# Kernel tuning notes

Measured on AMD Instinct MI355X. Metric: run time of the kernel, lower is better.

## Reference

```python
import jax, jax.numpy as jnp
import numpy as np

N_NODES = 50000
EPS_NORM = 1e-12
EPS_ENT = 1e-8

def _l2norm(x):
    # torch.nn.functional.normalize: x / clamp(||x||, min=1e-12)
    n = jnp.sqrt(jnp.sum(x * x, axis=-1, keepdims=True))
    return x / jnp.maximum(n, EPS_NORM)

def _layer(hidden, src, dst, edge_type, multi_emb, proto_emb):
    # hidden: [N,H]; multi_emb: [R,P,H]; proto_emb: [P,H]
    inp_j = hidden[src]                          # [E,H] gather
    rel_basis = multi_emb[edge_type]             # [E,P,H] gather
    sims = jnp.einsum('eh,ph->ep', _l2norm(inp_j), _l2norm(proto_emb))  # cosine sim [E,P]
    proto_proba = jax.nn.softmax(sims, axis=1)   # [E,P]
    msg = jnp.einsum('ep,eph->eh', proto_proba, rel_basis)              # [E,H]
    ent = -jnp.sum(proto_proba * jnp.log(proto_proba + EPS_ENT), axis=1)  # [E]
    logits = -ent
    # scatter_softmax over destination index
    seg_max = jax.ops.segment_max(logits, dst, num_segments=N_NODES)
    ex = jnp.exp(logits - seg_max[dst])
    denom = jax.ops.segment_sum(ex, dst, num_segments=N_NODES)
    attn = ex / denom[dst]                       # [E]
    out = jax.ops.segment_sum(attn[:, None] * msg, dst, num_segments=N_NODES)  # [N,H]
    return out

def setup_inputs() -> dict:
    key = jax.random.key(0)
    ks = jax.random.split(key, 6)
    E = 800000
    H, R, P, L = 128, 18, 18, 3  # num_layers=4 -> 3 NBFCluttr layers
    edge_index = jax.random.randint(ks[0], (2, E), 0, N_NODES, dtype=jnp.int64) if jax.config.read('jax_enable_x64') else jax.random.randint(ks[0], (2, E), 0, N_NODES, dtype=jnp.int32)
    edge_type = jax.random.randint(ks[1], (E,), 0, R, dtype=edge_index.dtype)
    tail_indices = jax.random.randint(ks[2], (1024,), 0, N_NODES, dtype=edge_index.dtype)
    multi_embeddings = jax.random.uniform(ks[3], (L, R, P, H), dtype=jnp.float32)
    proto_embeddings = jax.random.uniform(ks[4], (L, P, H), dtype=jnp.float32)
    source_embedding = jax.random.uniform(ks[5], (H,), dtype=jnp.float32)
    return {"edge_index": edge_index, "edge_type": edge_type, "tail_indices": tail_indices,
            "multi_embeddings": multi_embeddings, "proto_embeddings": proto_embeddings,
            "source_embedding": source_embedding}

def reference(edge_index, edge_type, tail_indices, multi_embeddings, proto_embeddings, source_embedding):
    src, dst = edge_index[0], edge_index[1]
    H = source_embedding.shape[0]
    # boundary condition: source node gets source_embedding, rest zero
    hidden = jnp.zeros((N_NODES, H), dtype=source_embedding.dtype).at[0].set(source_embedding)
    L = multi_embeddings.shape[0]
    for l in range(L):  # small fixed loop over structurally distinct layers
        hidden = _layer(hidden, src, dst, edge_type, multi_embeddings[l], proto_embeddings[l])
    # apply_classifier, eval_mode=True, use_mlp_classifier=False -> cosine sims to last layer prototypes
    out_emb = hidden[tail_indices]               # [B,H]
    sims = jnp.einsum('nh,ph->np', _l2norm(out_emb), _l2norm(proto_embeddings[-1]))
    return sims  # gumbel_softmax_sample with eval_mode=True returns logits unchanged
```

## Files before the change

### kernel.cpp

```cpp
#include <hip/hip_runtime.h>
#include <hip/hip_bf16.h>


#define N_NODES 50000
#define H 128
#define P 18
#define RP 324
#define KPAD 352
#define K0PAD 32
#define ELLW 64
#define NPART 8
#define NODES_PER_PART 6250
#define PREP_MAIN_BLOCKS 384
#define PREP_PN_BLOCKS 14
#define PREP_GS_BLOCKS 162
#define N0CAP 1024

typedef _Float16 half8 __attribute__((ext_vector_type(8)));
typedef _Float16 half2v __attribute__((ext_vector_type(2)));
typedef float floatx4 __attribute__((ext_vector_type(4)));

__global__ __launch_bounds__(256) void ell_kernel(const int* __restrict__ src,
                                                  const int* __restrict__ dst,
                                                  const int* __restrict__ etype,
                                                  unsigned* __restrict__ cur,
                                                  unsigned* __restrict__ ep,
                                                  unsigned* __restrict__ n0list, int E) {
  int part = blockIdx.x & (NPART - 1);
  int i = (blockIdx.x >> 3) * 256 + threadIdx.x;
  if (i >= E) return;
  int d = dst[i];
  int lo = part * NODES_PER_PART;
  if (d < lo || d >= lo + NODES_PER_PART) return;
  int s = src[i];
  int r = etype[i];
  unsigned pos = atomicAdd(&cur[d], 1u);
  if (pos < ELLW)
    ep[(size_t)d * ELLW + pos] = (unsigned)s | ((unsigned)r << 20);
  if (s == 0) {
    unsigned ix = atomicAdd(&cur[N_NODES], 1u);
    if (ix < N0CAP) n0list[ix] = (unsigned)d | ((unsigned)r << 20);
  }
}

__global__ __launch_bounds__(256) void prep_kernel(const float* __restrict__ multi,
                                                   const float* __restrict__ proto,
                                                   const float* __restrict__ semb,
                                                   float* __restrict__ pN,
                                                   _Float16* __restrict__ Btg,
                                                   _Float16* __restrict__ Btl0,
                                                   _Float16* __restrict__ BtD,
                                                   float* __restrict__ GS,
                                                   unsigned* __restrict__ cur) {
  int bid = blockIdx.x;
  if (bid >= PREP_MAIN_BLOCKS + PREP_PN_BLOCKS) {
    int wave = threadIdx.x >> 6, lane = threadIdx.x & 63;
    int pi = (bid - PREP_MAIN_BLOCKS - PREP_PN_BLOCKS) * 4 + wave;
    if (pi >= 648) return;
    float pr = 1.f / 18.f, ent0 = 0.f;
#pragma unroll
    for (int p = 0; p < P; p++) ent0 -= pr * __logf(pr + 1e-8f);
    float qc = __expf(-ent0) * pr;
    bool isG = pi < 324;
    int rr = isG ? pi / P : (pi - 324) / P;
    int cc = isG ? pi - rr * P : (pi - 324) - rr * P;
    float ca = 0.f, cb = 0.f;
#pragma unroll
    for (int q2 = 0; q2 < P; q2++) {
      ca += multi[(rr * P + q2) * H + lane];
      cb += multi[(rr * P + q2) * H + lane + 64];
    }
    ca *= qc; cb *= qc;
    float xa, xb, rn = 0.f;
    if (isG) {
      xa = proto[(P + cc) * H + lane];
      xb = proto[(P + cc) * H + lane + 64];
      rn = xa * xa + xb * xb;
    } else {
      xa = 0.f; xb = 0.f;
#pragma unroll
      for (int q2 = 0; q2 < P; q2++) {
        xa += multi[(cc * P + q2) * H + lane];
        xb += multi[(cc * P + q2) * H + lane + 64];
      }
      xa *= qc; xb *= qc;
    }
    float dotp = ca * xa + cb * xb;
    for (int m = 32; m > 0; m >>= 1) {
      dotp += __shfl_xor(dotp, m, 64);
      rn += __shfl_xor(rn, m, 64);
    }
    float val = isG ? dotp / fmaxf(sqrtf(rn), 1e-12f) : dotp;
    if (lane == 0) GS[pi] = val;
    return;
  }
  if (bid >= PREP_MAIN_BLOCKS) {
    int wave = threadIdx.x >> 6, l = threadIdx.x & 63;
    int row = (bid - PREP_MAIN_BLOCKS) * 4 + wave;
    if (row >= 54) return;
    float a = proto[row * H + l], b = proto[row * H + 64 + l];
    float ss = a * a + b * b;
    for (int m = 32; m > 0; m >>= 1) ss += __shfl_xor(ss, m, 64);
    float inv = 1.f / fmaxf(sqrtf(ss), 1e-12f);
    pN[row * H + l] = a * inv;
    pN[row * H + 64 + l] = b * inv;
    return;
  }
  int idx = bid * 256 + threadIdx.x;
  if (idx <= N_NODES) cur[idx] = 0u;
  if (idx < 2 * H * KPAD) {
    int l = idx / (H * KPAD), rem = idx - l * (H * KPAD);
    int h = rem / KPAD, k = rem - h * KPAD;
    const float* B = multi + (size_t)(l + 1) * RP * H;
    Btg[idx] = (k < RP) ? (_Float16)B[k * H + h] : (_Float16)0.f;
    return;
  }
  int idx2 = idx - 2 * H * KPAD;
  if (idx2 >= H * 64) return;
  int h = idx2 >> 6, k = idx2 & 63;
  float s0 = semb[k], s1 = semb[k + 64];
  float ssq = s0 * s0 + s1 * s1;
  float dq[P];
#pragma unroll
  for (int p = 0; p < P; p++) {
    float a = proto[p * H + k], b = proto[p * H + 64 + k];
    float rn = a * a + b * b;
    for (int m = 32; m > 0; m >>= 1) rn += __shfl_xor(rn, m, 64);
    float rinv = 1.f / fmaxf(sqrtf(rn), 1e-12f);
    dq[p] = (s0 * a + s1 * b) * rinv;
  }
  for (int m = 1; m <= 32; m <<= 1) {
    ssq += __shfl_xor(ssq, m, 64);
#pragma unroll
    for (int p = 0; p < P; p++) dq[p] += __shfl_xor(dq[p], m, 64);
  }
  float inv = 1.f / fmaxf(sqrtf(ssq), 1e-12f);
  float sum = 0.f;
#pragma unroll
  for (int p = 0; p < P; p++) {
    dq[p] = __expf(dq[p] * inv - 1.f);
    sum += dq[p];
  }
  float isum = 1.f / sum, ent = 0.f;
#pragma unroll
  for (int p = 0; p < P; p++) {
    dq[p] *= isum;
    ent -= dq[p] * __logf(dq[p] + 1e-8f);
  }
  float w = __expf(-ent);
  float pr = 1.f / 18.f, ent0 = 0.f;
#pragma unroll
  for (int p = 0; p < P; p++) ent0 -= pr * __logf(pr + 1e-8f);
  float qc = __expf(-ent0) * pr;
  if (k < K0PAD) {
    float v = 0.f;
    if (k < P) {
#pragma unroll
      for (int p = 0; p < P; p++) v += qc * multi[(k * P + p) * H + h];
    }
    Btl0[h * K0PAD + k] = (_Float16)v;
  } else if (k < K0PAD + P) {
    int r = k - K0PAD;
    float v = 0.f;
#pragma unroll
    for (int p = 0; p < P; p++) v += (w * dq[p] - qc) * multi[(r * P + p) * H + h];
    BtD[r * H + h] = (_Float16)v;
  }
}

__global__ __launch_bounds__(256) void histq_kernel(const unsigned* __restrict__ ep,
                                                    const unsigned* __restrict__ cur,
                                                    const float* __restrict__ GS,
                                                    _Float16* __restrict__ q, int n) {
  __shared__ float gs[648];
  for (int i = threadIdx.x; i < 648; i += 256) gs[i] = GS[i];
  __syncthreads();
  int wave = threadIdx.x >> 6, lane = threadIdx.x & 63;
  int nd = blockIdx.x * 4 + wave;
  if (nd >= n) return;
  int cnt = (int)cur[nd];
  if (cnt > ELLW) cnt = ELLW;
  bool a = lane < cnt;
  unsigned pk = a ? ep[(size_t)nd * ELLW + lane] : 0xFFFFFFFFu;
  int r = (int)(pk >> 20);
  float creg = 0.f;
#pragma unroll
  for (int rr = 0; rr < P; rr++) {
    unsigned long long m = __ballot(a && (r == rr));
    if (lane == rr) creg = (float)__popcll(m);
  }
  float dot = 0.f, t = 0.f;
#pragma unroll
  for (int rr = 0; rr < P; rr++) {
    float c = __shfl(creg, rr, 64);
    if (lane < P) {
      dot += c * gs[rr * P + lane];
      t += c * gs[324 + rr * P + lane];
    }
  }
  float u = (lane < P) ? creg * t : 0.f;
  for (int m = 1; m <= 16; m <<= 1) u += __shfl_xor(u, m, 32);
  float ss = u;
  float inv = 1.f / fmaxf(sqrtf(ss), 1e-12f);
  float e = (lane < P) ? __expf(dot * inv - 1.f) : 0.f;
  float sum = e;
  for (int m = 1; m <= 16; m <<= 1) sum += __shfl_xor(sum, m, 32);
  float prb = e / sum;
  float term = (lane < P) ? prb * __logf(prb + 1e-8f) : 0.f;
  float ent = term;
  for (int m = 1; m <= 16; m <<= 1) ent += __shfl_xor(ent, m, 32);
  float w = __expf(ent);
  if (lane < P) q[(size_t)nd * P + lane] = (_Float16)(w * prb);
}

__global__ __launch_bounds__(256) void patch_kernel(const unsigned* __restrict__ cur,
                                                    const unsigned* __restrict__ n0list,
                                                    const unsigned* __restrict__ ep,
                                                    const _Float16* __restrict__ Btl0,
                                                    const _Float16* __restrict__ BtD,
                                                    const float* __restrict__ pN,
                                                    _Float16* __restrict__ q) {
  int n0 = (int)cur[N_NODES];
  if (n0 > N0CAP) n0 = N0CAP;
  int wave = threadIdx.x >> 6, lane = threadIdx.x & 63;
  int e = blockIdx.x * 4 + wave;
  if (e >= n0) return;
  unsigned pe = n0list[e];
  int d = (int)(pe & 0xFFFFFu);
  for (int e2 = 0; e2 < e; e2++)
    if ((int)(n0list[e2] & 0xFFFFFu) == d) return;
  int cnt = (int)cur[d];
  if (cnt > ELLW) cnt = ELLW;
  bool a = lane < cnt;
  unsigned pk2 = a ? ep[(size_t)d * ELLW + lane] : 0xFFFFFFFFu;
  int rr0 = (int)(pk2 >> 20);
  float creg = 0.f;
#pragma unroll
  for (int rr = 0; rr < P; rr++) {
    unsigned long long m = __ballot(a && (rr0 == rr));
    if (lane == rr) creg = (float)__popcll(m);
  }
  float ya = 0.f, yb = 0.f;
#pragma unroll
  for (int rr = 0; rr < P; rr++) {
    float c = __shfl(creg, rr, 64);
    ya += c * (float)Btl0[lane * K0PAD + rr];
    yb += c * (float)Btl0[(lane + 64) * K0PAD + rr];
  }
  for (int e2 = e; e2 < n0; e2++) {
    unsigned p2 = n0list[e2];
    if ((int)(p2 & 0xFFFFFu) != d) continue;
    int r2 = (int)(p2 >> 20);
    ya += (float)BtD[r2 * H + lane];
    yb += (float)BtD[r2 * H + lane + 64];
  }
  float ss = ya * ya + yb * yb;
  float dot[P];
#pragma unroll
  for (int p = 0; p < P; p++) dot[p] = ya * pN[p * H + lane] + yb * pN[p * H + lane + 64];
  for (int m = 1; m <= 32; m <<= 1) {
    ss += __shfl_xor(ss, m, 64);
#pragma unroll
    for (int p = 0; p < P; p++) dot[p] += __shfl_xor(dot[p], m, 64);
  }
  float inv = 1.f / fmaxf(sqrtf(ss), 1e-12f);
  float sum = 0.f;
#pragma unroll
  for (int p = 0; p < P; p++) {
    dot[p] = __expf(dot[p] * inv - 1.f);
    sum += dot[p];
  }
  float isum = 1.f / sum, ent = 0.f;
#pragma unroll
  for (int p = 0; p < P; p++) {
    dot[p] *= isum;
    ent -= dot[p] * __logf(dot[p] + 1e-8f);
  }
  float w = __expf(-ent);
  if (lane < P) q[(size_t)d * P + lane] = (_Float16)(w * dot[lane]);
}

__global__ __launch_bounds__(256) void scatter_kernel(const unsigned* __restrict__ ep,
                                                      const unsigned* __restrict__ cur,
                                                      const _Float16* __restrict__ q,
                                                      const int* __restrict__ tl,
                                                      _Float16* __restrict__ M, int n) {
  __shared__ float sl[4][3 * RP];
  int wave = threadIdx.x >> 6, lane = threadIdx.x & 63;
  int t = blockIdx.x * 4 + wave;
  float* s0 = sl[wave];
  for (int i = lane; i < 3 * RP; i += 64) s0[i] = 0.f;
  int sub = lane / 18;
  int j = lane - sub * 18;
  bool act = (sub < 3) && (t < n);
  int cnt = 0;
  size_t b = 0;
  if (t < n) {
    int nd = tl ? tl[t] : t;
    b = (size_t)nd * ELLW;
    cnt = (int)cur[nd];
    if (cnt > ELLW) cnt = ELLW;
  }
  float* ms = s0 + (sub < 3 ? sub : 0) * RP;
  for (int it = 0; it < cnt; it += 18) {
    bool aa[6];
    unsigned pk[6];
    float qv[6];
#pragma unroll
    for (int u = 0; u < 6; u++) {
      int e = it + 3 * u + sub;
      aa[u] = act && (e < cnt);
      pk[u] = aa[u] ? ep[b + e] : 0u;
    }
#pragma unroll
    for (int u = 0; u < 6; u++)
      qv[u] = aa[u] ? (float)q[(size_t)(pk[u] & 0xFFFFFu) * P + j] : 0.f;
#pragma unroll
    for (int u = 0; u < 6; u++)
      if (aa[u]) ms[(pk[u] >> 20) * P + j] += qv[u];
  }
  if (t < n) {
    for (int wd = lane; wd < RP / 2; wd += 64) {
      float2 x0 = *(const float2*)(s0 + 2 * wd);
      float2 x1 = *(const float2*)(s0 + RP + 2 * wd);
      float2 x2 = *(const float2*)(s0 + 2 * RP + 2 * wd);
      half2v hv;
      hv[0] = (_Float16)(x0.x + x1.x + x2.x);
      hv[1] = (_Float16)(x0.y + x1.y + x2.y);
      *(half2v*)(M + (size_t)t * KPAD + 2 * wd) = hv;
    }
    for (int wd = RP / 2 + lane; wd < KPAD / 2; wd += 64) {
      half2v z = {};
      *(half2v*)(M + (size_t)t * KPAD + 2 * wd) = z;
    }
  }
}

template <int MODE>
__global__ __launch_bounds__(256) void gemm_kernel(const _Float16* __restrict__ M,
                                                   const _Float16* __restrict__ Bt,
                                                   const float* __restrict__ pN,
                                                   void* __restrict__ out_ptr, int n,
                                                   int kpad) {
  __shared__ float smem_f[64 * 132];
  _Float16* As = (_Float16*)smem_f;
  _Float16* Bs = (_Float16*)(smem_f + 1024);
  int tid = threadIdx.x;
  int wave = tid >> 6, lane = tid & 63;
  int m15 = lane & 15, quad = lane >> 4;
  int n0 = blockIdx.x * 64;
  floatx4 acc[4][2] = {};

  __shared__ float pns[4 * P * 36];
  for (int i = tid; i < 4 * P * 32; i += 256) {
    int s = i / (P * 32), r = i - s * (P * 32);
    int p = r >> 5, kk = r & 31;
    pns[s * (P * 36) + p * 36 + kk] = pN[p * H + s * 32 + kk];
  }

  for (int kt = 0; kt < (kpad >> 5); kt++) {
    int k0 = kt * 32;
    __syncthreads();
    {
      int row = tid >> 2, kc = (tid & 3) * 8;
      int gr = n0 + row;
      half8 v = {};
      if (gr < n) v = *(const half8*)(M + (size_t)gr * kpad + k0 + kc);
      *(half8*)(As + row * 32 + kc) = v;
    }
    {
      int col = tid >> 1, kc = (tid & 1) * 16;
      const _Float16* srcp = Bt + (size_t)col * kpad + k0 + kc;
      *(half8*)(Bs + col * 32 + kc) = *(const half8*)srcp;
      *(half8*)(Bs + col * 32 + kc + 8) = *(const half8*)(srcp + 8);
    }
    __syncthreads();
    half8 bfrag0 = *(const half8*)(Bs + (wave * 32 + m15) * 32 + quad * 8);
    half8 bfrag1 = *(const half8*)(Bs + (wave * 32 + 16 + m15) * 32 + quad * 8);
#pragma unroll
    for (int mt = 0; mt < 4; mt++) {
      half8 afrag = *(const half8*)(As + (mt * 16 + m15) * 32 + quad * 8);
      acc[mt][0] = __builtin_amdgcn_mfma_f32_16x16x32_f16(afrag, bfrag0, acc[mt][0], 0, 0, 0);
      acc[mt][1] = __builtin_amdgcn_mfma_f32_16x16x32_f16(afrag, bfrag1, acc[mt][1], 0, 0, 0);
    }
  }
  __syncthreads();
#pragma unroll
  for (int mt = 0; mt < 4; mt++)
#pragma unroll
    for (int c = 0; c < 2; c++)
#pragma unroll
      for (int reg = 0; reg < 4; reg++)
        smem_f[(mt * 16 + quad * 4 + reg) * 132 + wave * 32 + c * 16 + m15] = acc[mt][c][reg];
  __syncthreads();
  int node = tid >> 2, sub = tid & 3;
  int gnode = n0 + node;
  const float* trow = smem_f + node * 132 + sub * 32;
  const float* ps = pns + sub * (P * 36);
  float ss = 0.f;
  float dot[P];
#pragma unroll
  for (int p = 0; p < P; p++) dot[p] = 0.f;
#pragma unroll
  for (int k4 = 0; k4 < 8; k4++) {
    float4 y = *(const float4*)(trow + k4 * 4);
    ss += y.x * y.x + y.y * y.y + y.z * y.z + y.w * y.w;
#pragma unroll
    for (int p = 0; p < P; p++) {
      float4 b = *(const float4*)(ps + p * 36 + k4 * 4);
      dot[p] += y.x * b.x + y.y * b.y + y.z * b.z + y.w * b.w;
    }
  }
  for (int m = 1; m <= 2; m <<= 1) {
    ss += __shfl_xor(ss, m, 64);
#pragma unroll
    for (int p = 0; p < P; p++) dot[p] += __shfl_xor(dot[p], m, 64);
  }
  if (gnode < n) {
    float inv = 1.f / fmaxf(sqrtf(ss), 1e-12f);
    if (MODE == 1) {
      float* outp = (float*)out_ptr;
      for (int p = sub; p < P; p += 4) outp[(size_t)gnode * P + p] = dot[p] * inv;
    } else {
      float sum = 0.f;
#pragma unroll
      for (int p = 0; p < P; p++) {
        dot[p] = __expf(dot[p] * inv - 1.f);
        sum += dot[p];
      }
      float isum = 1.f / sum, ent = 0.f;
#pragma unroll
      for (int p = 0; p < P; p++) {
        dot[p] *= isum;
        ent -= dot[p] * __logf(dot[p] + 1e-8f);
      }
      float w = __expf(-ent);
      _Float16* qp = (_Float16*)out_ptr;
      for (int p = sub; p < P; p += 4) qp[(size_t)gnode * P + p] = (_Float16)(w * dot[p]);
    }
  }
}

extern "C" void kernel_launch(void* const* d_in, const int* in_sizes, int n_in,
                              void* d_out, int out_size, void* d_ws, size_t ws_size,
                              hipStream_t stream) {
  const int* eidx = (const int*)d_in[0];
  int E = in_sizes[0] / 2;
  const int* src = eidx;
  const int* dst = eidx + E;
  const int* etype = (const int*)d_in[1];
  const int* tails = (const int*)d_in[2];
  int T = in_sizes[2];
  const float* multi = (const float*)d_in[3];
  const float* proto = (const float*)d_in[4];
  const float* semb = (const float*)d_in[5];
  float* out = (float*)d_out;

  char* w = (char*)d_ws;
  auto alloc = [&](size_t bytes) {
    char* p = w;
    w += (bytes + 255) & ~(size_t)255;
    return p;
  };
  _Float16* q = (_Float16*)alloc((size_t)N_NODES * P * 2);
  float* pNs = (float*)alloc((size_t)3 * P * H * 4);
  float* GS = (float*)alloc((size_t)648 * 4);
  _Float16* Mg = (_Float16*)alloc((size_t)N_NODES * KPAD * 2);
  _Float16* Btg = (_Float16*)alloc((size_t)2 * H * KPAD * 2);
  _Float16* Btl0 = (_Float16*)alloc((size_t)H * K0PAD * 2);
  _Float16* BtD = (_Float16*)alloc((size_t)P * H * 2);
  unsigned* cur = (unsigned*)alloc((size_t)(N_NODES + 1) * 4);
  unsigned* n0list = (unsigned*)alloc((size_t)N0CAP * 4);
  unsigned* ep = (unsigned*)alloc((size_t)N_NODES * ELLW * 4);

  int eb = (E + 255) / 256;

  prep_kernel<<<PREP_MAIN_BLOCKS + PREP_PN_BLOCKS + PREP_GS_BLOCKS, 256, 0, stream>>>(
      multi, proto, semb, pNs, Btg, Btl0, BtD, GS, cur);

  ell_kernel<<<eb * NPART, 256, 0, stream>>>(src, dst, etype, cur, ep, n0list, E);

  histq_kernel<<<(N_NODES + 3) / 4, 256, 0, stream>>>(ep, cur, GS, q, N_NODES);
  patch_kernel<<<(N0CAP + 3) / 4, 256, 0, stream>>>(cur, n0list, ep, Btl0, BtD,
                                                    pNs + (size_t)1 * P * H, q);

  scatter_kernel<<<(N_NODES + 3) / 4, 256, 0, stream>>>(ep, cur, q, nullptr, Mg, N_NODES);
  gemm_kernel<0><<<(N_NODES + 63) / 64, 256, 0, stream>>>(Mg, Btg, pNs + (size_t)2 * P * H, q,
                                                          N_NODES, KPAD);

  scatter_kernel<<<(T + 3) / 4, 256, 0, stream>>>(ep, cur, q, tails, Mg, T);
  gemm_kernel<1><<<(T + 63) / 64, 256, 0, stream>>>(Mg, Btg + (size_t)H * KPAD,
                                                    pNs + (size_t)2 * P * H, out, T, KPAD);
}
```

Before: 230.9 us.

## Restrict penultimate layer to in-neighbors of tail nodes

Adds a need_kernel that marks and compacts the distinct source nodes feeding the tail nodes. The layer-2 scatter and GEMM then run only over that compacted list, with the GEMM writing q through an index map, instead of over all 50000 nodes. Effective sizes are read from a device counter, so blocks past the live count exit early. This cuts most of the full-graph scatter and GEMM work. In exchange it adds a small extra kernel with atomics, and it silently drops nodes if more than NEED_CAP distinct neighbors are needed.

```diff
diff --git a/kernel.cpp b/kernel.cpp
--- a/kernel.cpp
+++ b/kernel.cpp
@@ -15,6 +15,7 @@
 #define PREP_PN_BLOCKS 14
 #define PREP_GS_BLOCKS 162
 #define N0CAP 1024
+#define NEED_CAP 20480
 
 typedef _Float16 half8 __attribute__((ext_vector_type(8)));
 typedef _Float16 half2v __attribute__((ext_vector_type(2)));
@@ -43,6 +44,26 @@
   }
 }
 
+__global__ __launch_bounds__(256) void need_kernel(const int* __restrict__ tl,
+                                                   const unsigned* __restrict__ ep,
+                                                   unsigned* __restrict__ cur,
+                                                   unsigned* __restrict__ nflag,
+                                                   unsigned* __restrict__ needlist, int T) {
+  int wave = threadIdx.x >> 6, lane = threadIdx.x & 63;
+  int t = blockIdx.x * 4 + wave;
+  if (t >= T) return;
+  int nd = tl[t];
+  int cnt = (int)cur[nd];
+  if (cnt > ELLW) cnt = ELLW;
+  if (lane < cnt) {
+    unsigned s = ep[(size_t)nd * ELLW + lane] & 0xFFFFFu;
+    if (atomicExch(&nflag[s], 1u) == 0u) {
+      unsigned ix = atomicAdd(&cur[N_NODES + 1], 1u);
+      if (ix < NEED_CAP) needlist[ix] = s;
+    }
+  }
+}
+
 __global__ __launch_bounds__(256) void prep_kernel(const float* __restrict__ multi,
                                                    const float* __restrict__ proto,
                                                    const float* __restrict__ semb,
@@ -51,7 +72,8 @@
                                                    _Float16* __restrict__ Btl0,
                                                    _Float16* __restrict__ BtD,
                                                    float* __restrict__ GS,
-                                                   unsigned* __restrict__ cur) {
+                                                   unsigned* __restrict__ cur,
+                                                   unsigned* __restrict__ nflag) {
   int bid = blockIdx.x;
   if (bid >= PREP_MAIN_BLOCKS + PREP_PN_BLOCKS) {
     int wave = threadIdx.x >> 6, lane = threadIdx.x & 63;
@@ -107,7 +129,8 @@
     return;
   }
   int idx = bid * 256 + threadIdx.x;
-  if (idx <= N_NODES) cur[idx] = 0u;
+  if (idx <= N_NODES + 1) cur[idx] = 0u;
+  if (idx < N_NODES) nflag[idx] = 0u;
   if (idx < 2 * H * KPAD) {
     int l = idx / (H * KPAD), rem = idx - l * (H * KPAD);
     int h = rem / KPAD, k = rem - h * KPAD;
@@ -284,18 +307,24 @@
                                                       const unsigned* __restrict__ cur,
                                                       const _Float16* __restrict__ q,
                                                       const int* __restrict__ tl,
+                                                      const unsigned* __restrict__ dc,
                                                       _Float16* __restrict__ M, int n) {
   __shared__ float sl[4][3 * RP];
   int wave = threadIdx.x >> 6, lane = threadIdx.x & 63;
   int t = blockIdx.x * 4 + wave;
+  int neff = n;
+  if (dc) {
+    int c = (int)dc[0];
+    if (c < neff) neff = c;
+  }
   float* s0 = sl[wave];
   for (int i = lane; i < 3 * RP; i += 64) s0[i] = 0.f;
   int sub = lane / 18;
   int j = lane - sub * 18;
-  bool act = (sub < 3) && (t < n);
+  bool act = (sub < 3) && (t < neff);
   int cnt = 0;
   size_t b = 0;
-  if (t < n) {
+  if (t < neff) {
     int nd = tl ? tl[t] : t;
     b = (size_t)nd * ELLW;
     cnt = (int)cur[nd];
@@ -319,7 +348,7 @@
     for (int u = 0; u < 6; u++)
       if (aa[u]) ms[(pk[u] >> 20) * P + j] += qv[u];
   }
-  if (t < n) {
+  if (t < neff) {
     for (int wd = lane; wd < RP / 2; wd += 64) {
       float2 x0 = *(const float2*)(s0 + 2 * wd);
       float2 x1 = *(const float2*)(s0 + RP + 2 * wd);
@@ -340,15 +369,23 @@
 __global__ __launch_bounds__(256) void gemm_kernel(const _Float16* __restrict__ M,
                                                    const _Float16* __restrict__ Bt,
                                                    const float* __restrict__ pN,
+                                                   const int* __restrict__ map,
+                                                   const unsigned* __restrict__ dc,
                                                    void* __restrict__ out_ptr, int n,
                                                    int kpad) {
+  int neff = n;
+  if (dc) {
+    int c = (int)dc[0];
+    if (c < neff) neff = c;
+  }
+  int n0 = blockIdx.x * 64;
+  if (n0 >= neff) return;
   __shared__ float smem_f[64 * 132];
   _Float16* As = (_Float16*)smem_f;
   _Float16* Bs = (_Float16*)(smem_f + 1024);
   int tid = threadIdx.x;
   int wave = tid >> 6, lane = tid & 63;
   int m15 = lane & 15, quad = lane >> 4;
-  int n0 = blockIdx.x * 64;
   floatx4 acc[4][2] = {};
 
   __shared__ float pns[4 * P * 36];
@@ -365,7 +402,7 @@
       int row = tid >> 2, kc = (tid & 3) * 8;
       int gr = n0 + row;
       half8 v = {};
-      if (gr < n) v = *(const half8*)(M + (size_t)gr * kpad + k0 + kc);
+      if (gr < neff) v = *(const half8*)(M + (size_t)gr * kpad + k0 + kc);
       *(half8*)(As + row * 32 + kc) = v;
     }
     {
@@ -416,7 +453,7 @@
 #pragma unroll
     for (int p = 0; p < P; p++) dot[p] += __shfl_xor(dot[p], m, 64);
   }
-  if (gnode < n) {
+  if (gnode < neff) {
     float inv = 1.f / fmaxf(sqrtf(ss), 1e-12f);
     if (MODE == 1) {
       float* outp = (float*)out_ptr;
@@ -435,8 +472,9 @@
         ent -= dot[p] * __logf(dot[p] + 1e-8f);
       }
       float w = __expf(-ent);
+      int gout = map ? map[gnode] : gnode;
       _Float16* qp = (_Float16*)out_ptr;
-      for (int p = sub; p < P; p += 4) qp[(size_t)gnode * P + p] = (_Float16)(w * dot[p]);
+      for (int p = sub; p < P; p += 4) qp[(size_t)gout * P + p] = (_Float16)(w * dot[p]);
     }
   }
 }
@@ -469,14 +507,17 @@
   _Float16* Btg = (_Float16*)alloc((size_t)2 * H * KPAD * 2);
   _Float16* Btl0 = (_Float16*)alloc((size_t)H * K0PAD * 2);
   _Float16* BtD = (_Float16*)alloc((size_t)P * H * 2);
-  unsigned* cur = (unsigned*)alloc((size_t)(N_NODES + 1) * 4);
+  unsigned* cur = (unsigned*)alloc((size_t)(N_NODES + 2) * 4);
   unsigned* n0list = (unsigned*)alloc((size_t)N0CAP * 4);
+  unsigned* nflag = (unsigned*)alloc((size_t)N_NODES * 4);
+  unsigned* needlist = (unsigned*)alloc((size_t)NEED_CAP * 4);
   unsigned* ep = (unsigned*)alloc((size_t)N_NODES * ELLW * 4);
 
   int eb = (E + 255) / 256;
+  const unsigned* needcnt = cur + N_NODES + 1;
 
   prep_kernel<<<PREP_MAIN_BLOCKS + PREP_PN_BLOCKS + PREP_GS_BLOCKS, 256, 0, stream>>>(
-      multi, proto, semb, pNs, Btg, Btl0, BtD, GS, cur);
+      multi, proto, semb, pNs, Btg, Btl0, BtD, GS, cur, nflag);
 
   ell_kernel<<<eb * NPART, 256, 0, stream>>>(src, dst, etype, cur, ep, n0list, E);
 
@@ -484,11 +525,15 @@
   patch_kernel<<<(N0CAP + 3) / 4, 256, 0, stream>>>(cur, n0list, ep, Btl0, BtD,
                                                     pNs + (size_t)1 * P * H, q);
 
-  scatter_kernel<<<(N_NODES + 3) / 4, 256, 0, stream>>>(ep, cur, q, nullptr, Mg, N_NODES);
-  gemm_kernel<0><<<(N_NODES + 63) / 64, 256, 0, stream>>>(Mg, Btg, pNs + (size_t)2 * P * H, q,
-                                                          N_NODES, KPAD);
-
-  scatter_kernel<<<(T + 3) / 4, 256, 0, stream>>>(ep, cur, q, tails, Mg, T);
+  need_kernel<<<(T + 3) / 4, 256, 0, stream>>>(tails, ep, cur, nflag, needlist, T);
+
+  scatter_kernel<<<(NEED_CAP + 3) / 4, 256, 0, stream>>>(ep, cur, q, (const int*)needlist,
+                                                         needcnt, Mg, NEED_CAP);
+  gemm_kernel<0><<<(NEED_CAP + 63) / 64, 256, 0, stream>>>(
+      Mg, Btg, pNs + (size_t)2 * P * H, (const int*)needlist, needcnt, q, NEED_CAP, KPAD);
+
+  scatter_kernel<<<(T + 3) / 4, 256, 0, stream>>>(ep, cur, q, tails, nullptr, Mg, T);
   gemm_kernel<1><<<(T + 63) / 64, 256, 0, stream>>>(Mg, Btg + (size_t)H * KPAD,
-                                                    pNs + (size_t)2 * P * H, out, T, KPAD);
-}
+                                                    pNs + (size_t)2 * P * H, nullptr, nullptr,
+                                                    out, T, KPAD);
+}
```

New measurement: 214.3 us, median of 2. 7.2% less time.
